# Performance work log

Measured on AMD Instinct MI355X. Metric: run time of the kernel, lower is better.

## Reference

```python
import jax, jax.numpy as jnp
import numpy as np

EPS = 1e-8
TEMPERATURE = 1.0


def setup_inputs() -> dict:
    key = jax.random.key(0)
    basin_seq = jax.random.normal(key, (4, 512, 64), dtype=jnp.float32)
    residual_scale = jnp.ones((), dtype=jnp.float32)  # nn.Parameter(torch.tensor(1.0))
    return {"basin_seq": basin_seq, "residual_scale": residual_scale}


def _project_to_simplex(x):
    sp = jax.nn.softplus(x)
    p = sp / (sp.sum(axis=-1, keepdims=True) + EPS)
    return jnp.maximum(p, EPS)


def _qfi_attention_weights(x, temperature):
    # x: (B, T, D)
    p = _project_to_simplex(x)
    # fisher_rao_distance_simplex re-normalizes both operands
    p = p / (p.sum(axis=-1, keepdims=True) + EPS)
    # Faithful: eps is inside the sqrt, so this is a true (B,T,T,D) reduction,
    # not sqrt(p) @ sqrt(p)^T.
    inner = jnp.sqrt(p[:, :, None, :] * p[:, None, :, :] + EPS).sum(axis=-1)  # (B,T,T)
    inner = jnp.clip(inner, -1.0 + 1e-6, 1.0 - 1e-6)
    dist = 2.0 * jnp.arccos(inner)
    logits = -dist / max(float(temperature), 1e-6)
    return jax.nn.softmax(logits, axis=-1)  # (B,T,T)


def _phi_from_activations(acts):
    # acts: (B, T, D)
    t = acts.shape[1]
    x = acts - acts.mean(axis=1, keepdims=True)
    cov = jnp.einsum('btd,bte->bde', x, x) / (t + EPS)
    var = jnp.maximum(jnp.diagonal(cov, axis1=-2, axis2=-1), EPS)  # (B,D)
    denom = jnp.maximum(jnp.sqrt(var[:, :, None] * var[:, None, :]), EPS)
    corr = jnp.clip(cov / denom, -1.0, 1.0)
    d = corr.shape[-1]
    offdiag = corr * (1.0 - jnp.eye(d, dtype=corr.dtype))
    return jnp.abs(offdiag).mean(axis=(-2, -1))  # (B,)


def _kappa_proxy(x):
    return jnp.linalg.norm(x, axis=-1).mean(axis=-1)  # (B,)


def reference(basin_seq, residual_scale):
    x = basin_seq
    for _ in range(2):
        w = _qfi_attention_weights(x, TEMPERATURE)
        x_attn = jnp.einsum('bij,bjd->bid', w, x)
        x = 0.5 * x + 0.5 * x_attn
        x = x + 0.01 * residual_scale * (x_attn - x)
    phi = _phi_from_activations(x)
    kappa = _kappa_proxy(x)
    return (x, phi, kappa)
```

## Files before the change

kernel.cpp:

```cpp
#include <hip/hip_runtime.h>
#include <math.h>

#define B_ 4
#define T_ 512
#define D_ 64
#define EPS 1e-8f

__device__ __forceinline__ float wave_sum(float v) {
#pragma unroll
  for (int m = 1; m < 64; m <<= 1) v += __shfl_xor(v, m, 64);
  return v;
}
__device__ __forceinline__ float wave_max(float v) {
#pragma unroll
  for (int m = 1; m < 64; m <<= 1) v = fmaxf(v, __shfl_xor(v, m, 64));
  return v;
}
__device__ __forceinline__ float softplus_f(float x) {
  return fmaxf(x, 0.0f) + log1pf(expf(-fabsf(x)));
}
__device__ __forceinline__ float acos_fast(float x) {
  float r = fmaf(x, -0.0187293f, 0.0742610f);
  r = fmaf(r, x, -0.2121144f);
  r = fmaf(r, x, 1.5707288f);
  return r * sqrtf(1.0f - x);
}

__global__ __launch_bounds__(256) void proj_kernel(const float* __restrict__ x,
                                                   float* __restrict__ s) {
  int wave = threadIdx.x >> 6, lane = threadIdx.x & 63;
  int row = blockIdx.x * 4 + wave;
  float sp = softplus_f(x[row * D_ + lane]);
  float s1 = wave_sum(sp);
  float p = sp / (s1 + EPS);
  p = fmaxf(p, EPS);
  float s2 = wave_sum(p);
  s[row * D_ + lane] = sqrtf(p / (s2 + EPS));
}

__global__ __launch_bounds__(512) void logits_kernel(const float* __restrict__ s,
                                                     float* __restrict__ L) {
  int jt = blockIdx.x, it = blockIdx.y, b = blockIdx.z;
  __shared__ float si[64 * 68];
  __shared__ float sj[64 * 68];
  int tid = threadIdx.x;
  const float* sb = s + (size_t)b * T_ * D_;
#pragma unroll
  for (int k = 0; k < 2; ++k) {
    int idx = tid + k * 512;
    int row = idx >> 4, q = idx & 15;
    *(float4*)&si[row * 68 + q * 4] =
        *(const float4*)(sb + (it * 64 + row) * D_ + q * 4);
    *(float4*)&sj[row * 68 + q * 4] =
        *(const float4*)(sb + (jt * 64 + row) * D_ + q * 4);
  }
  __syncthreads();

  int dh = tid & 1, j4 = (tid >> 1) & 15, i4 = (tid >> 5) & 15;
  float acc[4][4];
#pragma unroll
  for (int a = 0; a < 4; ++a)
#pragma unroll
    for (int c = 0; c < 4; ++c) acc[a][c] = 0.f;

#pragma unroll
  for (int d4 = 0; d4 < 8; ++d4) {
    int db = dh * 32 + d4 * 4;
    float4 A[4], Bv[4];
#pragma unroll
    for (int a = 0; a < 4; ++a) A[a] = *(const float4*)&si[(i4 + 16 * a) * 68 + db];
#pragma unroll
    for (int c = 0; c < 4; ++c) Bv[c] = *(const float4*)&sj[(j4 + 16 * c) * 68 + db];
#pragma unroll
    for (int a = 0; a < 4; ++a)
#pragma unroll
      for (int c = 0; c < 4; ++c) {
        acc[a][c] = fmaf(A[a].x, Bv[c].x, acc[a][c]);
        acc[a][c] = fmaf(A[a].y, Bv[c].y, acc[a][c]);
        acc[a][c] = fmaf(A[a].z, Bv[c].z, acc[a][c]);
        acc[a][c] = fmaf(A[a].w, Bv[c].w, acc[a][c]);
      }
  }
#pragma unroll
  for (int a = 0; a < 4; ++a) {
    float* Lr = L + ((size_t)(b * T_) + it * 64 + i4 + 16 * a) * T_ + jt * 64;
#pragma unroll
    for (int c = 0; c < 4; ++c) {
      float v = acc[a][c] + __shfl_xor(acc[a][c], 1, 64);
      if (dh == 0) {
        float inner = fminf(fmaxf(v, 0.0f), 1.0f - 1e-6f);
        Lr[j4 + 16 * c] = -2.0f * acos_fast(inner);
      }
    }
  }
}

template <bool PART>
__global__ __launch_bounds__(512) void apply_kernel(
    const float* __restrict__ L, const float* __restrict__ xin,
    const float* __restrict__ rsp, float* __restrict__ xout,
    float* __restrict__ sout, float* __restrict__ covp,
    float* __restrict__ meanp, float* __restrict__ kappap) {
  int b = blockIdx.y, ic = blockIdx.x, i0 = ic * 8;
  __shared__ float wR[8 * 512];
  __shared__ float red[8 * 8 * 64];
  __shared__ float xf[8 * 68];
  __shared__ float kred[8];
  int tid = threadIdx.x;
  int w = tid >> 6, lane = tid & 63;

  {
    const float* Lr = L + ((size_t)(b * T_) + i0 + w) * T_;
    float4 v0 = ((const float4*)Lr)[lane];
    float4 v1 = ((const float4*)Lr)[64 + lane];
    float m = fmaxf(fmaxf(fmaxf(v0.x, v0.y), fmaxf(v0.z, v0.w)),
                    fmaxf(fmaxf(v1.x, v1.y), fmaxf(v1.z, v1.w)));
    m = wave_max(m);
    float4 e0, e1;
    e0.x = __expf(v0.x - m); e0.y = __expf(v0.y - m);
    e0.z = __expf(v0.z - m); e0.w = __expf(v0.w - m);
    e1.x = __expf(v1.x - m); e1.y = __expf(v1.y - m);
    e1.z = __expf(v1.z - m); e1.w = __expf(v1.w - m);
    float ssum = wave_sum(e0.x + e0.y + e0.z + e0.w + e1.x + e1.y + e1.z + e1.w);
    float inv = 1.0f / ssum;
    e0.x *= inv; e0.y *= inv; e0.z *= inv; e0.w *= inv;
    e1.x *= inv; e1.y *= inv; e1.z *= inv; e1.w *= inv;
    ((float4*)&wR[w * 512])[lane] = e0;
    ((float4*)&wR[w * 512])[64 + lane] = e1;
  }
  __syncthreads();

  int dg = tid & 15, js = tid >> 4;
  float acc[8][4];
#pragma unroll
  for (int i = 0; i < 8; ++i)
#pragma unroll
    for (int k = 0; k < 4; ++k) acc[i][k] = 0.f;
  const float* xb = xin + (size_t)(b * T_) * D_;
#pragma unroll
  for (int jj = 0; jj < 4; ++jj) {
    int jbase = js * 16 + jj * 4;
    float xr[4][4];
#pragma unroll
    for (int c = 0; c < 4; ++c) {
      float4 xv = *(const float4*)(xb + (jbase + c) * D_ + dg * 4);
      xr[c][0] = xv.x; xr[c][1] = xv.y; xr[c][2] = xv.z; xr[c][3] = xv.w;
    }
#pragma unroll
    for (int i = 0; i < 8; ++i) {
      float4 wv = *(const float4*)&wR[i * 512 + jbase];
      float wc[4] = {wv.x, wv.y, wv.z, wv.w};
#pragma unroll
      for (int c = 0; c < 4; ++c)
#pragma unroll
        for (int k = 0; k < 4; ++k)
          acc[i][k] = fmaf(wc[c], xr[c][k], acc[i][k]);
    }
  }
#pragma unroll
  for (int i = 0; i < 8; ++i)
#pragma unroll
    for (int k = 0; k < 4; ++k) {
      float v = acc[i][k];
      v += __shfl_xor(v, 16, 64);
      v += __shfl_xor(v, 32, 64);
      acc[i][k] = v;
    }
  if (lane < 16) {
#pragma unroll
    for (int i = 0; i < 8; ++i)
      *(float4*)&red[(w * 8 + i) * 64 + lane * 4] =
          make_float4(acc[i][0], acc[i][1], acc[i][2], acc[i][3]);
  }
  __syncthreads();

  float c01 = 0.01f * rsp[0];
  {
    int i = w, d = lane;
    float xa = 0.f;
#pragma unroll
    for (int ww = 0; ww < 8; ++ww) xa += red[(ww * 8 + i) * 64 + d];
    size_t idx = ((size_t)(b * T_) + i0 + i) * D_ + d;
    float xn = 0.5f * (1.0f - c01) * xin[idx] + 0.5f * (1.0f + c01) * xa;
    xout[idx] = xn;
    if (!PART) {
      float sp = softplus_f(xn);
      float s1 = wave_sum(sp);
      float p = sp / (s1 + EPS);
      p = fmaxf(p, EPS);
      float s2 = wave_sum(p);
      sout[idx] = sqrtf(p / (s2 + EPS));
    } else {
      xf[i * 68 + d] = xn;
      float ssq = wave_sum(xn * xn);
      if (lane == 0) kred[w] = sqrtf(ssq);
    }
  }
  if (PART) {
    __syncthreads();
    int dd = tid >> 3, e8 = tid & 7;
    float ac[8];
#pragma unroll
    for (int k = 0; k < 8; ++k) ac[k] = 0.f;
#pragma unroll
    for (int t = 0; t < 8; ++t) {
      float xd = xf[t * 68 + dd];
      const float4* te = (const float4*)&xf[t * 68 + e8 * 8];
      float4 v0 = te[0], v1 = te[1];
      ac[0] = fmaf(xd, v0.x, ac[0]); ac[1] = fmaf(xd, v0.y, ac[1]);
      ac[2] = fmaf(xd, v0.z, ac[2]); ac[3] = fmaf(xd, v0.w, ac[3]);
      ac[4] = fmaf(xd, v1.x, ac[4]); ac[5] = fmaf(xd, v1.y, ac[5]);
      ac[6] = fmaf(xd, v1.z, ac[6]); ac[7] = fmaf(xd, v1.w, ac[7]);
    }
    float* cp = covp + ((size_t)(b * 64 + ic)) * 4096 + dd * 64 + e8 * 8;
    *(float4*)cp = make_float4(ac[0], ac[1], ac[2], ac[3]);
    *(float4*)(cp + 4) = make_float4(ac[4], ac[5], ac[6], ac[7]);
    if (tid < 64) {
      float m = 0.f;
#pragma unroll
      for (int t = 0; t < 8; ++t) m += xf[t * 68 + tid];
      meanp[(b * 64 + ic) * 64 + tid] = m;
    }
    if (tid == 0) {
      float kk = 0.f;
#pragma unroll
      for (int ww = 0; ww < 8; ++ww) kk += kred[ww];
      kappap[b * 64 + ic] = kk;
    }
  }
}

__global__ __launch_bounds__(256) void p2a_kernel(
    const float* __restrict__ covp, const float* __restrict__ meanp,
    const float* __restrict__ kappap, float* __restrict__ covq,
    float* __restrict__ meanq, float* __restrict__ kappaq) {
  int blk = blockIdx.x;
  int b = blk >> 3, g = blk & 7;
  int tid = threadIdx.x;
  int dd = tid >> 2, e16 = tid & 3;
  float ac[16];
#pragma unroll
  for (int k = 0; k < 16; ++k) ac[k] = 0.f;
#pragma unroll
  for (int s = 0; s < 8; ++s) {
    const float* cp =
        covp + ((size_t)(b * 64 + g * 8 + s)) * 4096 + dd * 64 + e16 * 16;
#pragma unroll
    for (int kk = 0; kk < 4; ++kk) {
      float4 v = *(const float4*)(cp + kk * 4);
      ac[kk * 4] += v.x; ac[kk * 4 + 1] += v.y;
      ac[kk * 4 + 2] += v.z; ac[kk * 4 + 3] += v.w;
    }
  }
  float* cq = covq + (size_t)blk * 4096 + dd * 64 + e16 * 16;
#pragma unroll
  for (int kk = 0; kk < 4; ++kk)
    *(float4*)(cq + kk * 4) =
        make_float4(ac[kk * 4], ac[kk * 4 + 1], ac[kk * 4 + 2], ac[kk * 4 + 3]);
  if (tid < 64) {
    float m = 0.f;
#pragma unroll
    for (int s = 0; s < 8; ++s) m += meanp[(b * 64 + g * 8 + s) * 64 + tid];
    meanq[blk * 64 + tid] = m;
  }
  if (tid == 0) {
    float k = 0.f;
#pragma unroll
    for (int s = 0; s < 8; ++s) k += kappap[b * 64 + g * 8 + s];
    kappaq[blk] = k;
  }
}

__global__ __launch_bounds__(256) void p2b_kernel(
    const float* __restrict__ covq, const float* __restrict__ meanq,
    const float* __restrict__ kappaq, float* __restrict__ out) {
  int b = blockIdx.x;
  __shared__ float mu[64];
  __shared__ float var[64];
  __shared__ float phired[4];
  int tid = threadIdx.x;
  if (tid < 64) {
    float m = 0.f;
#pragma unroll
    for (int s = 0; s < 8; ++s) m += meanq[(b * 8 + s) * 64 + tid];
    mu[tid] = m * (1.0f / 512.0f);
  }
  __syncthreads();

  int dd = tid >> 2, e16 = tid & 3;
  float acc[16];
#pragma unroll
  for (int k = 0; k < 16; ++k) acc[k] = 0.f;
#pragma unroll
  for (int s = 0; s < 8; ++s) {
    const float* cp = covq + ((size_t)(b * 8 + s)) * 4096 + dd * 64 + e16 * 16;
#pragma unroll
    for (int kk = 0; kk < 4; ++kk) {
      float4 v = *(const float4*)(cp + kk * 4);
      acc[kk * 4] += v.x; acc[kk * 4 + 1] += v.y;
      acc[kk * 4 + 2] += v.z; acc[kk * 4 + 3] += v.w;
    }
  }
  float mud = mu[dd];
#pragma unroll
  for (int k = 0; k < 16; ++k)
    acc[k] = acc[k] * (1.0f / 512.0f) - mud * mu[e16 * 16 + k];
  if ((dd >> 4) == e16) var[dd] = fmaxf(acc[dd & 15], EPS);
  __syncthreads();

  float vd = var[dd];
  float psum = 0.f;
#pragma unroll
  for (int k = 0; k < 16; ++k) {
    int e = e16 * 16 + k;
    if (e == dd) continue;
    float denom = fmaxf(sqrtf(vd * var[e]), EPS);
    float cc = fminf(fmaxf(acc[k] / denom, -1.0f), 1.0f);
    psum += fabsf(cc);
  }
  psum = wave_sum(psum);
  if ((tid & 63) == 0) phired[tid >> 6] = psum;
  __syncthreads();
  if (tid == 0) {
    out[B_ * T_ * D_ + b] = (phired[0] + phired[1] + phired[2] + phired[3]) *
                            (1.0f / 4096.0f);
    float ks = 0.f;
#pragma unroll
    for (int s = 0; s < 8; ++s) ks += kappaq[b * 8 + s];
    out[B_ * T_ * D_ + B_ + b] = ks * (1.0f / 512.0f);
  }
}

extern "C" void kernel_launch(void* const* d_in, const int* in_sizes, int n_in,
                              void* d_out, int out_size, void* d_ws, size_t ws_size,
                              hipStream_t stream) {
  const float* x0 = (const float*)d_in[0];
  const float* rs = (const float*)d_in[1];
  float* out = (float*)d_out;
  float* s = (float*)d_ws;
  float* s2 = s + 131072;
  float* x1 = s2 + 131072;
  float* L = x1 + 131072;
  float* covp = L + 1048576;
  float* meanp = covp + 256 * 4096;
  float* kappap = meanp + 16384;
  float* covq = kappap + 256;
  float* meanq = covq + 32 * 4096;
  float* kappaq = meanq + 2048;

  dim3 lgrd(8, 8, B_), agrd(64, B_);
  proj_kernel<<<(B_ * T_) / 4, 256, 0, stream>>>(x0, s);
  logits_kernel<<<lgrd, 512, 0, stream>>>(s, L);
  apply_kernel<false><<<agrd, 512, 0, stream>>>(L, x0, rs, x1, s2, covp, meanp, kappap);
  logits_kernel<<<lgrd, 512, 0, stream>>>(s2, L);
  apply_kernel<true><<<agrd, 512, 0, stream>>>(L, x1, rs, out, s, covp, meanp, kappap);
  p2a_kernel<<<32, 256, 0, stream>>>(covp, meanp, kappap, covq, meanq, kappaq);
  p2b_kernel<<<B_, 256, 0, stream>>>(covq, meanq, kappaq, out);
}
```

Baseline: 106.0 us.

## Fuse simplex projection into logits kernel and merge final reduction kernels

```diff
diff --git a/kernel.cpp b/kernel.cpp
--- a/kernel.cpp
+++ b/kernel.cpp
@@ -17,7 +17,7 @@
   return v;
 }
 __device__ __forceinline__ float softplus_f(float x) {
-  return fmaxf(x, 0.0f) + log1pf(expf(-fabsf(x)));
+  return fmaxf(x, 0.0f) + __logf(1.0f + __expf(-fabsf(x)));
 }
 __device__ __forceinline__ float acos_fast(float x) {
   float r = fmaf(x, -0.0187293f, 0.0742610f);
@@ -26,33 +26,57 @@
   return r * sqrtf(1.0f - x);
 }
 
-__global__ __launch_bounds__(256) void proj_kernel(const float* __restrict__ x,
-                                                   float* __restrict__ s) {
-  int wave = threadIdx.x >> 6, lane = threadIdx.x & 63;
-  int row = blockIdx.x * 4 + wave;
-  float sp = softplus_f(x[row * D_ + lane]);
-  float s1 = wave_sum(sp);
-  float p = sp / (s1 + EPS);
-  p = fmaxf(p, EPS);
-  float s2 = wave_sum(p);
-  s[row * D_ + lane] = sqrtf(p / (s2 + EPS));
-}
-
-__global__ __launch_bounds__(512) void logits_kernel(const float* __restrict__ s,
+template <bool COMPUTE_S>
+__global__ __launch_bounds__(512) void logits_kernel(const float* __restrict__ xs,
                                                      float* __restrict__ L) {
   int jt = blockIdx.x, it = blockIdx.y, b = blockIdx.z;
   __shared__ float si[64 * 68];
   __shared__ float sj[64 * 68];
   int tid = threadIdx.x;
-  const float* sb = s + (size_t)b * T_ * D_;
-#pragma unroll
-  for (int k = 0; k < 2; ++k) {
-    int idx = tid + k * 512;
-    int row = idx >> 4, q = idx & 15;
-    *(float4*)&si[row * 68 + q * 4] =
-        *(const float4*)(sb + (it * 64 + row) * D_ + q * 4);
-    *(float4*)&sj[row * 68 + q * 4] =
-        *(const float4*)(sb + (jt * 64 + row) * D_ + q * 4);
+  const float* sb = xs + (size_t)b * T_ * D_;
+
+  if (COMPUTE_S) {
+    int row = tid >> 2, q = tid & 3;
+    int grow = (row < 64) ? (it * 64 + row) : (jt * 64 + (row - 64));
+    const float4* xr = (const float4*)(sb + grow * D_ + q * 16);
+    float sp[16];
+    float4 v0 = xr[0], v1 = xr[1], v2 = xr[2], v3 = xr[3];
+    sp[0] = softplus_f(v0.x); sp[1] = softplus_f(v0.y);
+    sp[2] = softplus_f(v0.z); sp[3] = softplus_f(v0.w);
+    sp[4] = softplus_f(v1.x); sp[5] = softplus_f(v1.y);
+    sp[6] = softplus_f(v1.z); sp[7] = softplus_f(v1.w);
+    sp[8] = softplus_f(v2.x); sp[9] = softplus_f(v2.y);
+    sp[10] = softplus_f(v2.z); sp[11] = softplus_f(v2.w);
+    sp[12] = softplus_f(v3.x); sp[13] = softplus_f(v3.y);
+    sp[14] = softplus_f(v3.z); sp[15] = softplus_f(v3.w);
+    float r1 = 0.f;
+#pragma unroll
+    for (int k = 0; k < 16; ++k) r1 += sp[k];
+    r1 += __shfl_xor(r1, 1, 64);
+    r1 += __shfl_xor(r1, 2, 64);
+    float inv1 = 1.0f / (r1 + EPS);
+    float r2 = 0.f;
+#pragma unroll
+    for (int k = 0; k < 16; ++k) {
+      sp[k] = fmaxf(sp[k] * inv1, EPS);
+      r2 += sp[k];
+    }
+    r2 += __shfl_xor(r2, 1, 64);
+    r2 += __shfl_xor(r2, 2, 64);
+    float inv2 = 1.0f / (r2 + EPS);
+    float* dst = (row < 64) ? &si[row * 68 + q * 16] : &sj[(row - 64) * 68 + q * 16];
+#pragma unroll
+    for (int k = 0; k < 16; ++k) dst[k] = sqrtf(sp[k] * inv2);
+  } else {
+#pragma unroll
+    for (int k = 0; k < 2; ++k) {
+      int idx = tid + k * 512;
+      int row = idx >> 4, q = idx & 15;
+      *(float4*)&si[row * 68 + q * 4] =
+          *(const float4*)(sb + (it * 64 + row) * D_ + q * 4);
+      *(float4*)&sj[row * 68 + q * 4] =
+          *(const float4*)(sb + (jt * 64 + row) * D_ + q * 4);
+    }
   }
   __syncthreads();
 
@@ -230,50 +254,10 @@
   }
 }
 
-__global__ __launch_bounds__(256) void p2a_kernel(
-    const float* __restrict__ covp, const float* __restrict__ meanp,
-    const float* __restrict__ kappap, float* __restrict__ covq,
-    float* __restrict__ meanq, float* __restrict__ kappaq) {
-  int blk = blockIdx.x;
-  int b = blk >> 3, g = blk & 7;
-  int tid = threadIdx.x;
-  int dd = tid >> 2, e16 = tid & 3;
-  float ac[16];
-#pragma unroll
-  for (int k = 0; k < 16; ++k) ac[k] = 0.f;
-#pragma unroll
-  for (int s = 0; s < 8; ++s) {
-    const float* cp =
-        covp + ((size_t)(b * 64 + g * 8 + s)) * 4096 + dd * 64 + e16 * 16;
-#pragma unroll
-    for (int kk = 0; kk < 4; ++kk) {
-      float4 v = *(const float4*)(cp + kk * 4);
-      ac[kk * 4] += v.x; ac[kk * 4 + 1] += v.y;
-      ac[kk * 4 + 2] += v.z; ac[kk * 4 + 3] += v.w;
-    }
-  }
-  float* cq = covq + (size_t)blk * 4096 + dd * 64 + e16 * 16;
-#pragma unroll
-  for (int kk = 0; kk < 4; ++kk)
-    *(float4*)(cq + kk * 4) =
-        make_float4(ac[kk * 4], ac[kk * 4 + 1], ac[kk * 4 + 2], ac[kk * 4 + 3]);
-  if (tid < 64) {
-    float m = 0.f;
-#pragma unroll
-    for (int s = 0; s < 8; ++s) m += meanp[(b * 64 + g * 8 + s) * 64 + tid];
-    meanq[blk * 64 + tid] = m;
-  }
-  if (tid == 0) {
-    float k = 0.f;
-#pragma unroll
-    for (int s = 0; s < 8; ++s) k += kappap[b * 64 + g * 8 + s];
-    kappaq[blk] = k;
-  }
-}
-
-__global__ __launch_bounds__(256) void p2b_kernel(
-    const float* __restrict__ covq, const float* __restrict__ meanq,
-    const float* __restrict__ kappaq, float* __restrict__ out) {
+__global__ __launch_bounds__(256) void p2_kernel(const float* __restrict__ covp,
+                                                 const float* __restrict__ meanp,
+                                                 const float* __restrict__ kappap,
+                                                 float* __restrict__ out) {
   int b = blockIdx.x;
   __shared__ float mu[64];
   __shared__ float var[64];
@@ -281,8 +265,7 @@
   int tid = threadIdx.x;
   if (tid < 64) {
     float m = 0.f;
-#pragma unroll
-    for (int s = 0; s < 8; ++s) m += meanq[(b * 8 + s) * 64 + tid];
+    for (int s = 0; s < 64; ++s) m += meanp[(b * 64 + s) * 64 + tid];
     mu[tid] = m * (1.0f / 512.0f);
   }
   __syncthreads();
@@ -291,9 +274,8 @@
   float acc[16];
 #pragma unroll
   for (int k = 0; k < 16; ++k) acc[k] = 0.f;
-#pragma unroll
-  for (int s = 0; s < 8; ++s) {
-    const float* cp = covq + ((size_t)(b * 8 + s)) * 4096 + dd * 64 + e16 * 16;
+  for (int s = 0; s < 64; ++s) {
+    const float* cp = covp + ((size_t)(b * 64 + s)) * 4096 + dd * 64 + e16 * 16;
 #pragma unroll
     for (int kk = 0; kk < 4; ++kk) {
       float4 v = *(const float4*)(cp + kk * 4);
@@ -325,8 +307,7 @@
     out[B_ * T_ * D_ + b] = (phired[0] + phired[1] + phired[2] + phired[3]) *
                             (1.0f / 4096.0f);
     float ks = 0.f;
-#pragma unroll
-    for (int s = 0; s < 8; ++s) ks += kappaq[b * 8 + s];
+    for (int s = 0; s < 64; ++s) ks += kappap[b * 64 + s];
     out[B_ * T_ * D_ + B_ + b] = ks * (1.0f / 512.0f);
   }
 }
@@ -337,23 +318,17 @@
   const float* x0 = (const float*)d_in[0];
   const float* rs = (const float*)d_in[1];
   float* out = (float*)d_out;
-  float* s = (float*)d_ws;
-  float* s2 = s + 131072;
+  float* s2 = (float*)d_ws;
   float* x1 = s2 + 131072;
   float* L = x1 + 131072;
   float* covp = L + 1048576;
   float* meanp = covp + 256 * 4096;
   float* kappap = meanp + 16384;
-  float* covq = kappap + 256;
-  float* meanq = covq + 32 * 4096;
-  float* kappaq = meanq + 2048;
 
   dim3 lgrd(8, 8, B_), agrd(64, B_);
-  proj_kernel<<<(B_ * T_) / 4, 256, 0, stream>>>(x0, s);
-  logits_kernel<<<lgrd, 512, 0, stream>>>(s, L);
+  logits_kernel<true><<<lgrd, 512, 0, stream>>>(x0, L);
   apply_kernel<false><<<agrd, 512, 0, stream>>>(L, x0, rs, x1, s2, covp, meanp, kappap);
-  logits_kernel<<<lgrd, 512, 0, stream>>>(s2, L);
-  apply_kernel<true><<<agrd, 512, 0, stream>>>(L, x1, rs, out, s, covp, meanp, kappap);
-  p2a_kernel<<<32, 256, 0, stream>>>(covp, meanp, kappap, covq, meanq, kappaq);
-  p2b_kernel<<<B_, 256, 0, stream>>>(covq, meanq, kappaq, out);
-}
+  logits_kernel<false><<<lgrd, 512, 0, stream>>>(s2, L);
+  apply_kernel<true><<<agrd, 512, 0, stream>>>(L, x1, rs, out, s2, covp, meanp, kappap);
+  p2_kernel<<<B_, 256, 0, stream>>>(covp, meanp, kappap, out);
+}
```

New measurement: 121.9 us. +15.0%, slower.
